# Optimization experiments

Hardware: AMD Instinct MI355X
Metric: run time of the kernel (lower is better)

The kernel has to match this reference:

```python
import jax, jax.numpy as jnp
import numpy as np

B, S, D = 2, 1024, 1024
L, E, F = 2, 8, 2048


def setup_inputs() -> dict:
    key = jax.random.key(0)
    kx, kp, k1, k2 = jax.random.split(key, 4)
    x = jax.random.normal(kx, (B, S, D), dtype=jnp.float32)
    # prototypes scaled so dot products are O(1), keeping softmax well-behaved
    protos = jax.random.normal(kp, (L, E, D), dtype=jnp.float32) / np.sqrt(D)
    W1 = jax.random.normal(k1, (L, E, D, F), dtype=jnp.float32) * 0.02
    W2 = jax.random.normal(k2, (L, E, F, D), dtype=jnp.float32) * 0.02
    return {"x": x, "protos": protos, "W1": W1, "W2": W2, "k": 2}


def _route(x, protos_l, k):
    # expert_mapping: abs(dot(prototype, input)) per expert, keep top-k, rest -> -inf, softmax
    scores = jnp.abs(jnp.einsum("bsd,ed->bse", x, protos_l))  # [B,S,E]
    topv, _ = jax.lax.top_k(scores, k)
    thresh = topv[..., -1:]  # k-th largest per token
    masked = jnp.where(scores >= thresh, scores, -jnp.inf)
    return jax.nn.softmax(masked, axis=-1)  # [B,S,E]


def reference(x, protos, W1, W2, k):
    n_layers = protos.shape[0]
    for l in range(n_layers):  # fixed small layer loop
        w = _route(x, protos[l], k)  # [B,S,E]
        h = jax.nn.relu(jnp.einsum("bsd,edf->bsef", x, W1[l]))  # [B,S,E,F]
        y = jnp.einsum("bsef,efd,bse->bsd", h, W2[l], w)  # weighted expert mix
        x = x + y
    return x
```

## Files before the change

kernel.cpp:

```cpp
#include <hip/hip_runtime.h>
#include <hip/hip_bf16.h>
#include <cstdint>

#define T_TOKENS 2048
#define DDIM 1024
#define FDIM 2048
#define NEXP 8
#define BMPAD 64
#define RMAX 4608
#define RALLOC 4736

#define ATILE_EL 2048
#define BTILE_EL 4096
#define WLDP 132

typedef unsigned short u16;
typedef short bf16x8 __attribute__((ext_vector_type(8)));
typedef u16 u16x8 __attribute__((ext_vector_type(8)));
typedef u16 u16x4v __attribute__((ext_vector_type(4)));
typedef float f32x4 __attribute__((ext_vector_type(4)));

#define VMCNT(n) asm volatile("s_waitcnt vmcnt(" #n ")" ::: "memory")
#define SB() __builtin_amdgcn_sched_barrier(0)
#define BAR() __builtin_amdgcn_s_barrier()

__device__ __forceinline__ u16 bf16_rn(float f) {
  unsigned u = __builtin_bit_cast(unsigned, f);
  u += 0x7fffu + ((u >> 16) & 1u);
  return (u16)(u >> 16);
}
__device__ __forceinline__ float bf16_f(u16 h) {
  unsigned u = ((unsigned)h) << 16;
  return __builtin_bit_cast(float, u);
}
__device__ __forceinline__ void gl16(const void* g, void* l) {
  __builtin_amdgcn_global_load_lds((const __attribute__((address_space(1))) void*)g,
                                   (__attribute__((address_space(3))) void*)l, 16, 0, 0);
}

template <int GX, int GY, int GZ>
__device__ __forceinline__ void swz3(unsigned lin, int& bx, int& by, int& bz) {
  constexpr unsigned nwg = (unsigned)GX * GY * GZ;
  const unsigned nl = (lin & 7u) * (nwg >> 3) + (lin >> 3);
  bx = nl % GX;
  const unsigned t = nl / GX;
  by = t % GY;
  bz = t / GY;
}


__device__ __forceinline__ void route_dev(
    int t, const float* __restrict__ x, const float* __restrict__ protos,
    int* __restrict__ eid, float* __restrict__ wgt, float* red) {
  const int tid = threadIdx.x;
  const float4 xv = ((const float4*)(x + (size_t)t * DDIM))[tid];
  float acc[NEXP];
#pragma unroll
  for (int e = 0; e < NEXP; ++e) {
    const float4 p = ((const float4*)protos)[e * 256 + tid];
    acc[e] = xv.x * p.x + xv.y * p.y + xv.z * p.z + xv.w * p.w;
  }
#pragma unroll
  for (int e = 0; e < NEXP; ++e) red[e * 256 + tid] = acc[e];
  __syncthreads();
  for (int s = 128; s > 0; s >>= 1) {
    if (tid < s) {
#pragma unroll
      for (int e = 0; e < NEXP; ++e) red[e * 256 + tid] += red[e * 256 + tid + s];
    }
    __syncthreads();
  }
  if (tid == 0) {
    float m1 = -1.f, m2 = -1.f;
    int i1 = 0, i2 = 0;
#pragma unroll
    for (int e = 0; e < NEXP; ++e) {
      float s = fabsf(red[e * 256]);
      if (s > m1) { m2 = m1; i2 = i1; m1 = s; i1 = e; }
      else if (s > m2) { m2 = s; i2 = e; }
    }
    float e2 = __expf(m2 - m1);
    float z = 1.f + e2;
    eid[t * 2] = i1;
    eid[t * 2 + 1] = i2;
    wgt[t * 2] = 1.f / z;
    wgt[t * 2 + 1] = e2 / z;
  }
}

template <bool LO>
__device__ __forceinline__ void wconv_dev(
    int nb, int kb, int e, const float* __restrict__ W, u16* __restrict__ Hi,
    u16* __restrict__ Lo, int K, int N, float* tile) {
  const float* Wp = W + ((size_t)e * K + (size_t)kb * 32) * N + nb * 128;
  const int t = threadIdx.x;
#pragma unroll
  for (int i = 0; i < 4; ++i) {
    const int f4 = i * 256 + t;
    const int kr = f4 >> 5;
    const int c4 = (f4 & 31) * 4;
    float4 v = *(const float4*)(Wp + (size_t)kr * N + c4);
    *(float4*)&tile[kr * WLDP + c4] = v;
  }
  __syncthreads();
  const size_t tb = (((size_t)e * (N >> 7) + nb) * (K >> 5) + kb) * BTILE_EL;
#pragma unroll
  for (int j = 0; j < 2; ++j) {
    const int cid = j * 256 + t;
    const int n = cid & 127, ksel = cid >> 7;
    u16x8 hv, lv;
#pragma unroll
    for (int i = 0; i < 8; ++i) {
      float f = tile[(ksel * 8 + i) * WLDP + n];
      u16 h = bf16_rn(f);
      hv[i] = h;
      if (LO) lv[i] = bf16_rn(f - bf16_f(h));
    }
    *(u16x8*)(Hi + tb + (size_t)cid * 8) = hv;
    if (LO) *(u16x8*)(Lo + tb + (size_t)cid * 8) = lv;
  }
}

__device__ __forceinline__ void wconv_p_dev(
    int nb, int kb, int e, const float* __restrict__ W, u16* __restrict__ Hi,
    const float* __restrict__ proto2, float* __restrict__ Ppart, int K, int N,
    float* smem) {
  float* tile = smem;
  float* pr = smem + 32 * WLDP;
  const float* Wp = W + ((size_t)e * K + (size_t)kb * 32) * N + nb * 128;
  const int t = threadIdx.x;
#pragma unroll
  for (int i = 0; i < 4; ++i) {
    const int f4 = i * 256 + t;
    const int kr = f4 >> 5;
    const int c4 = (f4 & 31) * 4;
    float4 v = *(const float4*)(Wp + (size_t)kr * N + c4);
    *(float4*)&tile[kr * WLDP + c4] = v;
  }
  {
    const int idx = t * 4;
    const int e2 = idx >> 7, n = idx & 127;
    *(float4*)&pr[e2 * 128 + n] =
        *(const float4*)(proto2 + (size_t)e2 * DDIM + nb * 128 + n);
  }
  __syncthreads();
  const size_t tb = (((size_t)e * (N >> 7) + nb) * (K >> 5) + kb) * BTILE_EL;
#pragma unroll
  for (int j = 0; j < 2; ++j) {
    const int cid = j * 256 + t;
    const int n = cid & 127, ksel = cid >> 7;
    u16x8 hv;
#pragma unroll
    for (int i = 0; i < 8; ++i) hv[i] = bf16_rn(tile[(ksel * 8 + i) * WLDP + n]);
    *(u16x8*)(Hi + tb + (size_t)cid * 8) = hv;
  }
  const int e2 = t >> 5, f = t & 31;
  float s = 0.f;
#pragma unroll
  for (int ii = 0; ii < 32; ++ii) {
    const int n4 = ((ii + f) & 31) * 4;
    const float4 tv = *(const float4*)&tile[f * WLDP + n4];
    const float4 pv = *(const float4*)&pr[e2 * 128 + n4];
    s += tv.x * pv.x + tv.y * pv.y + tv.z * pv.z + tv.w * pv.w;
  }
  Ppart[(((size_t)nb * NEXP + e) * NEXP + e2) * FDIM + kb * 32 + f] = s;
}

template <bool LO>
__device__ __forceinline__ void gather_dev(
    int r, const float* __restrict__ x, const int* __restrict__ row2token,
    u16* __restrict__ Ahi, u16* __restrict__ Alo) {
  const int t = row2token[r];
  const int c = threadIdx.x * 4;
  float4 v = make_float4(0.f, 0.f, 0.f, 0.f);
  if (t >= 0) v = *(const float4*)(x + (size_t)t * DDIM + c);
  float vv[4] = {v.x, v.y, v.z, v.w};
  u16x4v hi, lo;
#pragma unroll
  for (int i = 0; i < 4; ++i) {
    u16 h = bf16_rn(vv[i]);
    hi[i] = h;
    if (LO) lo[i] = bf16_rn(vv[i] - bf16_f(h));
  }
  const size_t el = ((size_t)(r >> 6) * (DDIM >> 5) + (c >> 5)) * ATILE_EL +
                    (size_t)(((c >> 3) & 3) * 64 + (r & 63)) * 8 + (c & 7);
  *(u16x4v*)(Ahi + el) = hi;
  if (LO) *(u16x4v*)(Alo + el) = lo;
}

__device__ __forceinline__ void route2_dev(
    int t, const float* __restrict__ x, const float* __restrict__ protos2,
    const u16* __restrict__ h_hi, const u16* __restrict__ h_lo,
    const float* __restrict__ P, const int* __restrict__ eidA,
    const int* __restrict__ pos, const float* __restrict__ wgtA,
    int* __restrict__ eidB, float* __restrict__ wgtB, float* red) {
  const int tid = threadIdx.x;
  const float4 xv = ((const float4*)(x + (size_t)t * DDIM))[tid];
  float acc[NEXP];
#pragma unroll
  for (int e = 0; e < NEXP; ++e) {
    const float4 p = ((const float4*)protos2)[e * 256 + tid];
    acc[e] = xv.x * p.x + xv.y * p.y + xv.z * p.z + xv.w * p.w;
  }
  const int p0 = pos[t * 2], p1 = pos[t * 2 + 1];
  const int e0 = eidA[t * 2], e1 = eidA[t * 2 + 1];
  const float w0 = wgtA[t * 2], w1 = wgtA[t * 2 + 1];
  const int f0 = tid * 8;
  const int nkbF = FDIM >> 5;
  float h0[8], h1[8];
  {
    const size_t el0 = ((size_t)(p0 >> 6) * nkbF + (f0 >> 5)) * ATILE_EL +
                       (size_t)((((f0 >> 3) & 3) * 64 + (p0 & 63)) * 8);
    const size_t el1 = ((size_t)(p1 >> 6) * nkbF + (f0 >> 5)) * ATILE_EL +
                       (size_t)((((f0 >> 3) & 3) * 64 + (p1 & 63)) * 8);
    u16x8 a = *(const u16x8*)&h_hi[el0], b = *(const u16x8*)&h_lo[el0];
    u16x8 c = *(const u16x8*)&h_hi[el1], d = *(const u16x8*)&h_lo[el1];
#pragma unroll
    for (int j = 0; j < 8; ++j) {
      h0[j] = bf16_f(a[j]) + bf16_f(b[j]);
      h1[j] = bf16_f(c[j]) + bf16_f(d[j]);
    }
  }
#pragma unroll
  for (int e2 = 0; e2 < NEXP; ++e2) {
    const float* P0 = P + ((size_t)(e0 * NEXP + e2)) * FDIM + f0;
    const float* P1 = P + ((size_t)(e1 * NEXP + e2)) * FDIM + f0;
    float c = 0.f;
#pragma unroll
    for (int j = 0; j < 8; ++j) c += w0 * h0[j] * P0[j] + w1 * h1[j] * P1[j];
    acc[e2] += c;
  }
#pragma unroll
  for (int e = 0; e < NEXP; ++e) red[e * 256 + tid] = acc[e];
  __syncthreads();
  for (int s = 128; s > 0; s >>= 1) {
    if (tid < s) {
#pragma unroll
      for (int e = 0; e < NEXP; ++e) red[e * 256 + tid] += red[e * 256 + tid + s];
    }
    __syncthreads();
  }
  if (tid == 0) {
    float m1 = -1.f, m2 = -1.f;
    int i1 = 0, i2 = 0;
#pragma unroll
    for (int e = 0; e < NEXP; ++e) {
      float s = fabsf(red[e * 256]);
      if (s > m1) { m2 = m1; i2 = i1; m1 = s; i1 = e; }
      else if (s > m2) { m2 = s; i2 = e; }
    }
    float e2 = __expf(m2 - m1);
    float z = 1.f + e2;
    eidB[t * 2] = i1;
    eidB[t * 2 + 1] = i2;
    wgtB[t * 2] = 1.f / z;
    wgtB[t * 2 + 1] = e2 / z;
  }
}

__device__ __forceinline__ void gemm_split_dev(
    unsigned lin, u16* lds, const u16* __restrict__ Ahi, const u16* __restrict__ Alo,
    const u16* __restrict__ Bhi, const u16* __restrict__ Blo,
    u16* __restrict__ OutHi, u16* __restrict__ OutLo,
    const int* __restrict__ cnt, const int* __restrict__ offp, int K, int N) {
  int bx, by, bz;
  swz3<FDIM / 128, RMAX / 64, NEXP>(lin, bx, by, bz);
  const int e = bz;
  const int cp = (cnt[e] + 63) & ~63;
  if (by * 64 >= cp) return;
  const int row0 = offp[e] + by * 64;
  const int n0 = bx * 128;
  const int nkb = K >> 5;
  constexpr int BUF_EL = 12288;

  const int tid = threadIdx.x;
  const int lane = tid & 63;
  const int wid = tid >> 6;
  const int wr = wid >> 1, wc = wid & 1;
  const int lr = lane & 15, kg = lane >> 4;
  const int lo16 = lane << 4;

  f32x4 acc[2][4];
#pragma unroll
  for (int i = 0; i < 2; ++i)
#pragma unroll
    for (int j = 0; j < 4; ++j)
#pragma unroll
      for (int r = 0; r < 4; ++r) acc[i][j][r] = 0.f;

  const size_t abase = (size_t)(row0 >> 6) * nkb;
  const size_t bbase = ((size_t)e * (N >> 7) + (n0 >> 7)) * nkb;

  auto STAGE = [&](int kb, int b) {
    char* d = (char*)(lds + b * BUF_EL);
    const char* gah = (const char*)(Ahi + (abase + kb) * ATILE_EL);
    const char* gal = (const char*)(Alo + (abase + kb) * ATILE_EL);
    const char* gbh = (const char*)(Bhi + (bbase + kb) * BTILE_EL);
    const char* gbl = (const char*)(Blo + (bbase + kb) * BTILE_EL);
    if (wid == 0) {
      gl16(gah + 0 * 1024 + lo16, d + 0 * 1024);
      gl16(gah + 1 * 1024 + lo16, d + 1 * 1024);
      gl16(gah + 2 * 1024 + lo16, d + 2 * 1024);
      gl16(gah + 3 * 1024 + lo16, d + 3 * 1024);
      gl16(gal + 0 * 1024 + lo16, d + 4096 + 0 * 1024);
      gl16(gal + 1 * 1024 + lo16, d + 4096 + 1 * 1024);
    } else if (wid == 1) {
      gl16(gal + 2 * 1024 + lo16, d + 4096 + 2 * 1024);
      gl16(gal + 3 * 1024 + lo16, d + 4096 + 3 * 1024);
      gl16(gbh + 0 * 1024 + lo16, d + 8192 + 0 * 1024);
      gl16(gbh + 1 * 1024 + lo16, d + 8192 + 1 * 1024);
      gl16(gbh + 2 * 1024 + lo16, d + 8192 + 2 * 1024);
      gl16(gbh + 3 * 1024 + lo16, d + 8192 + 3 * 1024);
    } else if (wid == 2) {
      gl16(gbh + 4 * 1024 + lo16, d + 8192 + 4 * 1024);
      gl16(gbh + 5 * 1024 + lo16, d + 8192 + 5 * 1024);
      gl16(gbh + 6 * 1024 + lo16, d + 8192 + 6 * 1024);
      gl16(gbh + 7 * 1024 + lo16, d + 8192 + 7 * 1024);
      gl16(gbl + 0 * 1024 + lo16, d + 16384 + 0 * 1024);
      gl16(gbl + 1 * 1024 + lo16, d + 16384 + 1 * 1024);
    } else {
      gl16(gbl + 2 * 1024 + lo16, d + 16384 + 2 * 1024);
      gl16(gbl + 3 * 1024 + lo16, d + 16384 + 3 * 1024);
      gl16(gbl + 4 * 1024 + lo16, d + 16384 + 4 * 1024);
      gl16(gbl + 5 * 1024 + lo16, d + 16384 + 5 * 1024);
      gl16(gbl + 6 * 1024 + lo16, d + 16384 + 6 * 1024);
      gl16(gbl + 7 * 1024 + lo16, d + 16384 + 7 * 1024);
    }
  };

  STAGE(0, 0);
  int cur = 0;
  for (int kb = 0; kb < nkb; ++kb) {
    const bool pf = (kb + 1 < nkb);
    if (pf) STAGE(kb + 1, cur ^ 1);
    if (pf) { VMCNT(6); } else { VMCNT(0); }
    SB(); BAR(); SB();

    const u16* buf = lds + cur * BUF_EL;
    const u16* AsH = buf;
    const u16* AsL = buf + 2048;
    const u16* BsH = buf + 4096;
    const u16* BsL = buf + 8192;
    const int arow = (kg * 64 + wr * 32 + lr) * 8;
    const int bcol = (kg * 128 + wc * 64 + lr) * 8;

    bf16x8 ah0 = *(const bf16x8*)&AsH[arow];
    bf16x8 ah1 = *(const bf16x8*)&AsH[arow + 128];
    bf16x8 bh[4];
#pragma unroll
    for (int j = 0; j < 4; ++j) bh[j] = *(const bf16x8*)&BsH[bcol + j * 128];
#pragma unroll
    for (int j = 0; j < 4; ++j) {
      acc[0][j] = __builtin_amdgcn_mfma_f32_16x16x32_bf16(ah0, bh[j], acc[0][j], 0, 0, 0);
      acc[1][j] = __builtin_amdgcn_mfma_f32_16x16x32_bf16(ah1, bh[j], acc[1][j], 0, 0, 0);
    }
    bf16x8 al0 = *(const bf16x8*)&AsL[arow];
    bf16x8 al1 = *(const bf16x8*)&AsL[arow + 128];
#pragma unroll
    for (int j = 0; j < 4; ++j) {
      bf16x8 bl = *(const bf16x8*)&BsL[bcol + j * 128];
      acc[0][j] = __builtin_amdgcn_mfma_f32_16x16x32_bf16(ah0, bl, acc[0][j], 0, 0, 0);
      acc[1][j] = __builtin_amdgcn_mfma_f32_16x16x32_bf16(ah1, bl, acc[1][j], 0, 0, 0);
      acc[0][j] = __builtin_amdgcn_mfma_f32_16x16x32_bf16(al0, bh[j], acc[0][j], 0, 0, 0);
      acc[1][j] = __builtin_amdgcn_mfma_f32_16x16x32_bf16(al1, bh[j], acc[1][j], 0, 0, 0);
    }
    SB(); BAR(); SB();
    cur ^= 1;
  }

  const int nkbO = N >> 5;
#pragma unroll
  for (int i = 0; i < 2; ++i) {
#pragma unroll
    for (int j = 0; j < 4; ++j) {
      const int Cj = n0 + wc * 64 + j * 16 + lr;
      f32x4 v = acc[i][j];
#pragma unroll
      for (int r = 0; r < 4; ++r) {
        const int R = row0 + wr * 32 + i * 16 + kg * 4 + r;
        float f = fmaxf(v[r], 0.f);
        const size_t el = ((size_t)(R >> 6) * nkbO + (Cj >> 5)) * ATILE_EL +
                          (size_t)(((Cj >> 3) & 3) * 64 + (R & 63)) * 8 + (Cj & 7);
        u16 h = bf16_rn(f);
        OutHi[el] = h;
        OutLo[el] = bf16_rn(f - bf16_f(h));
      }
    }
  }
}

template <int GX, int GY, bool RELU, int OUTMODE>
__device__ __forceinline__ void gemm_plain_dev(
    unsigned lin, u16* lds, const u16* __restrict__ Ahi, const u16* __restrict__ Bhi,
    u16* __restrict__ OutHi, float* __restrict__ OutF,
    const int* __restrict__ cnt, const int* __restrict__ offp, int K, int N) {
  int bx, by, bz;
  swz3<GX, GY, NEXP>(lin, bx, by, bz);
  const int e = bz;
  const int cp = (cnt[e] + 63) & ~63;
  if (by * 128 >= cp) return;
  const int row0 = offp[e] + by * 128;
  const int rend = offp[e] + cp;
  const int n0 = bx * 128;
  const int nkb = K >> 5;
  constexpr int BUF_EL = 8192;

  const int tid = threadIdx.x;
  const int lane = tid & 63;
  const int wid = tid >> 6;
  const int wr = wid >> 1, wc = wid & 1;
  const int lr = lane & 15, kg = lane >> 4;
  const int lo16 = lane << 4;

  f32x4 acc[4][4];
#pragma unroll
  for (int i = 0; i < 4; ++i)
#pragma unroll
    for (int j = 0; j < 4; ++j)
#pragma unroll
      for (int r = 0; r < 4; ++r) acc[i][j][r] = 0.f;

  const int at0 = row0 >> 6;
  const size_t bbase = ((size_t)e * (N >> 7) + (n0 >> 7)) * nkb;

  auto STAGE = [&](int kb, int b) {
    char* d = (char*)(lds + b * BUF_EL);
    if (wid < 2) {
      const char* g = (const char*)(Ahi + ((size_t)(at0 + wid) * nkb + kb) * ATILE_EL);
      gl16(g + 0 * 1024 + lo16, d + wid * 4096 + 0 * 1024);
      gl16(g + 1 * 1024 + lo16, d + wid * 4096 + 1 * 1024);
      gl16(g + 2 * 1024 + lo16, d + wid * 4096 + 2 * 1024);
      gl16(g + 3 * 1024 + lo16, d + wid * 4096 + 3 * 1024);
    } else {
      const char* g = (const char*)(Bhi + (bbase + kb) * BTILE_EL) + (wid - 2) * 4096;
      gl16(g + 0 * 1024 + lo16, d + 8192 + (wid - 2) * 4096 + 0 * 1024);
      gl16(g + 1 * 1024 + lo16, d + 8192 + (wid - 2) * 4096 + 1 * 1024);
      gl16(g + 2 * 1024 + lo16, d + 8192 + (wid - 2) * 4096 + 2 * 1024);
      gl16(g + 3 * 1024 + lo16, d + 8192 + (wid - 2) * 4096 + 3 * 1024);
    }
  };

  STAGE(0, 0);
  int cur = 0;
  for (int kb = 0; kb < nkb; ++kb) {
    const bool pf = (kb + 1 < nkb);
    if (pf) STAGE(kb + 1, cur ^ 1);
    if (pf) { VMCNT(4); } else { VMCNT(0); }
    SB(); BAR(); SB();

    const u16* buf = lds + cur * BUF_EL;
    const u16* AsH = buf + wr * 2048;
    const u16* BsH = buf + 4096;
    const int arow = (kg * 64 + lr) * 8;
    const int bcol = (kg * 128 + wc * 64 + lr) * 8;

    bf16x8 ah[4], bh[4];
#pragma unroll
    for (int i = 0; i < 4; ++i) ah[i] = *(const bf16x8*)&AsH[arow + i * 128];
#pragma unroll
    for (int j = 0; j < 4; ++j) bh[j] = *(const bf16x8*)&BsH[bcol + j * 128];
#pragma unroll
    for (int i = 0; i < 4; ++i)
#pragma unroll
      for (int j = 0; j < 4; ++j)
        acc[i][j] = __builtin_amdgcn_mfma_f32_16x16x32_bf16(ah[i], bh[j], acc[i][j], 0, 0, 0);
    SB(); BAR(); SB();
    cur ^= 1;
  }

  const int nkbO = N >> 5;
#pragma unroll
  for (int i = 0; i < 4; ++i) {
#pragma unroll
    for (int j = 0; j < 4; ++j) {
      const int Cj = n0 + wc * 64 + j * 16 + lr;
      f32x4 v = acc[i][j];
#pragma unroll
      for (int r = 0; r < 4; ++r) {
        const int R = row0 + wr * 64 + i * 16 + kg * 4 + r;
        if (R >= rend) continue;
        float f = v[r];
        if (RELU) f = fmaxf(f, 0.f);
        if constexpr (OUTMODE == 0) {
          OutF[(size_t)R * N + Cj] = f;
        } else {
          const size_t el = ((size_t)(R >> 6) * nkbO + (Cj >> 5)) * ATILE_EL +
                            (size_t)(((Cj >> 3) & 3) * 64 + (R & 63)) * 8 + (Cj & 7);
          OutHi[el] = bf16_rn(f);
        }
      }
    }
  }
}

__device__ __forceinline__ void compact_dev(
    const int* __restrict__ eid, int* __restrict__ cnt, int* __restrict__ offp,
    int* __restrict__ row2token, int* __restrict__ pos, int* lcnt) {
  int* s_off = lcnt + NEXP * 256;
  int* s_tot = s_off + NEXP;
  const int tid = threadIdx.x;
  const int base = tid * 16;
  int my[16];
#pragma unroll
  for (int i = 0; i < 4; ++i)
    *(int4*)&my[i * 4] = *(const int4*)(eid + base + i * 4);
#pragma unroll
  for (int e = 0; e < NEXP; ++e) {
    int c = 0;
#pragma unroll
    for (int i = 0; i < 16; ++i) c += (my[i] == e) ? 1 : 0;
    lcnt[e * 256 + tid] = c;
  }
  for (int r = tid; r < RMAX; r += 256) row2token[r] = -1;
  __syncthreads();
  if (tid < NEXP) {
    int run = 0;
    for (int i = 0; i < 256; ++i) {
      int v = lcnt[tid * 256 + i];
      lcnt[tid * 256 + i] = run;
      run += v;
    }
    s_tot[tid] = run;
  }
  __syncthreads();
  if (tid == 0) {
    int o = 0;
    for (int e = 0; e < NEXP; ++e) {
      s_off[e] = o;
      o += (s_tot[e] + BMPAD - 1) & ~(BMPAD - 1);
    }
  }
  __syncthreads();
  int myoff[NEXP];
#pragma unroll
  for (int e = 0; e < NEXP; ++e) myoff[e] = s_off[e] + lcnt[e * 256 + tid];
#pragma unroll
  for (int i = 0; i < 16; ++i) {
    int r = 0;
#pragma unroll
    for (int e = 0; e < NEXP; ++e) r = (my[i] == e) ? myoff[e] : r;
    row2token[r] = (base + i) >> 1;
    pos[base + i] = r;
#pragma unroll
    for (int e = 0; e < NEXP; ++e) myoff[e] += (my[i] == e) ? 1 : 0;
  }
  if (tid < NEXP) {
    cnt[tid] = s_tot[tid];
    offp[tid] = s_off[tid];
  }
}


__global__ __launch_bounds__(256) void fusedK1_kernel(
    const float* __restrict__ xin, const float* __restrict__ protos,
    int* __restrict__ eidA, float* __restrict__ wgtA,
    const float* __restrict__ W2, u16* __restrict__ W2A,
    const float* __restrict__ proto2, float* __restrict__ Ppart,
    const float* __restrict__ W1, u16* __restrict__ W_hi, u16* __restrict__ W_lo) {
  __shared__ float smem[32 * WLDP + 8 * 128];
  const unsigned lin = blockIdx.x;
  if (lin < 2048u) {
    route_dev((int)lin, xin, protos, eidA, wgtA, smem);
  } else if (lin < 6144u) {
    const unsigned l2 = lin - 2048u;
    wconv_p_dev(l2 % 8, (l2 / 8) % 64, l2 / 512, W2, W2A, proto2, Ppart,
                FDIM, DDIM, smem);
  } else {
    const unsigned l3 = lin - 6144u;
    wconv_dev<true>(l3 % 16, (l3 / 16) % 32, l3 / 512, W1, W_hi, W_lo,
                    DDIM, FDIM, smem);
  }
}

__global__ __launch_bounds__(256) void compact_kernel(
    const int* __restrict__ eid, int* __restrict__ cnt, int* __restrict__ offp,
    int* __restrict__ row2token, int* __restrict__ pos) {
  __shared__ int lcnt[NEXP * 256 + 16];
  compact_dev(eid, cnt, offp, row2token, pos, lcnt);
}

__global__ __launch_bounds__(256) void fusedK3_kernel(
    const float* __restrict__ xin, const int* __restrict__ row2token,
    u16* __restrict__ Ag_hi, u16* __restrict__ Ag_lo,
    const float* __restrict__ Ppart, float* __restrict__ P) {
  const unsigned lin = blockIdx.x;
  if (lin < (unsigned)RMAX) {
    gather_dev<true>((int)lin, xin, row2token, Ag_hi, Ag_lo);
  } else {
    const int i = (int)(lin - RMAX) * 256 + threadIdx.x;
    float s = 0.f;
#pragma unroll
    for (int nb = 0; nb < 8; ++nb) s += Ppart[(size_t)nb * (NEXP * NEXP * FDIM) + i];
    P[i] = s;
  }
}

__global__ __launch_bounds__(256, 3) void fusedC2_kernel(
    const u16* __restrict__ Ag_hi, const u16* __restrict__ Ag_lo,
    const u16* __restrict__ W_hi, const u16* __restrict__ W_lo,
    u16* __restrict__ h_hi, u16* __restrict__ h_lo,
    const int* __restrict__ cnt, const int* __restrict__ offp) {
  __shared__ u16 lds[2 * 12288];
  gemm_split_dev(blockIdx.x, lds, Ag_hi, Ag_lo, W_hi, W_lo, h_hi, h_lo, cnt, offp,
                 DDIM, FDIM);
}

__global__ __launch_bounds__(256, 4) void fusedC3_kernel(
    const u16* __restrict__ h_hi, const u16* __restrict__ h_lo,
    const u16* __restrict__ W2A,
    float* __restrict__ part, const int* __restrict__ cnt, const int* __restrict__ offp,
    const float* __restrict__ W1b, u16* __restrict__ W_lo,
    const float* __restrict__ W2b, u16* __restrict__ W_hi,
    const float* __restrict__ xin, const float* __restrict__ protos2,
    const float* __restrict__ P, const int* __restrict__ eidA,
    const int* __restrict__ posA, const float* __restrict__ wgtA,
    int* __restrict__ eidB, float* __restrict__ wgtB) {
  __shared__ u16 lds[2 * 8192];
  const unsigned lin = blockIdx.x;
  if (lin < 2304u) {
    gemm_plain_dev<DDIM / 128, RMAX / 128, false, 0>(
        lin, lds, h_hi, W2A, nullptr, part, cnt, offp, FDIM, DDIM);
  } else if (lin < 6400u) {
    const unsigned l2 = lin - 2304u;
    wconv_dev<false>(l2 % 16, (l2 / 16) % 32, l2 / 512, W1b, W_lo, nullptr,
                     DDIM, FDIM, (float*)lds);
  } else if (lin < 10496u) {
    const unsigned l2 = lin - 6400u;
    wconv_dev<false>(l2 % 8, (l2 / 8) % 64, l2 / 512, W2b, W_hi, nullptr,
                     FDIM, DDIM, (float*)lds);
  } else {
    route2_dev((int)(lin - 10496u), xin, protos2, h_hi, h_lo, P, eidA, posA, wgtA,
               eidB, wgtB, (float*)lds);
  }
}

__global__ __launch_bounds__(256) void fusedD_kernel(
    const float* __restrict__ part, const int* __restrict__ pos,
    const float* __restrict__ wgt, const float* __restrict__ xin,
    float* __restrict__ xcur,
    const int* __restrict__ eidB, int* __restrict__ cnt, int* __restrict__ offp,
    int* __restrict__ row2token, int* __restrict__ posB) {
  __shared__ int lcnt[NEXP * 256 + 16];
  const unsigned lin = blockIdx.x;
  if (lin < 2048u) {
    const int t = lin;
    const int c = threadIdx.x * 4;
    const int p0 = pos[t * 2], p1 = pos[t * 2 + 1];
    const float w0 = wgt[t * 2], w1 = wgt[t * 2 + 1];
    float4 xa = *(const float4*)(xin + (size_t)t * DDIM + c);
    const float4 y0 = *(const float4*)(part + (size_t)p0 * DDIM + c);
    const float4 y1 = *(const float4*)(part + (size_t)p1 * DDIM + c);
    xa.x += w0 * y0.x + w1 * y1.x;
    xa.y += w0 * y0.y + w1 * y1.y;
    xa.z += w0 * y0.z + w1 * y1.z;
    xa.w += w0 * y0.w + w1 * y1.w;
    *(float4*)(xcur + (size_t)t * DDIM + c) = xa;
  } else {
    compact_dev(eidB, cnt, offp, row2token, posB, lcnt);
  }
}

__global__ __launch_bounds__(256) void gather_kernel(
    const float* __restrict__ x, const int* __restrict__ row2token,
    u16* __restrict__ Ahi) {
  gather_dev<false>(blockIdx.x, x, row2token, Ahi, nullptr);
}

template <int GX, bool RELU, int OUTMODE>
__global__ __launch_bounds__(256, 4) void gemm_plain_kernel(
    const u16* __restrict__ Ahi, const u16* __restrict__ Bhi,
    u16* __restrict__ OutHi, float* __restrict__ OutF,
    const int* __restrict__ cnt, const int* __restrict__ offp, int K, int N) {
  __shared__ u16 lds[2 * 8192];
  gemm_plain_dev<GX, RMAX / 128, RELU, OUTMODE>(blockIdx.x, lds, Ahi, Bhi, OutHi,
                                                OutF, cnt, offp, K, N);
}

__global__ __launch_bounds__(256) void apply_kernel(
    const float* __restrict__ part, const int* __restrict__ pos,
    const float* __restrict__ wgt, float* __restrict__ x) {
  const int t = blockIdx.x;
  const int c = threadIdx.x * 4;
  const int p0 = pos[t * 2], p1 = pos[t * 2 + 1];
  const float w0 = wgt[t * 2], w1 = wgt[t * 2 + 1];
  float4 xa = *(float4*)(x + (size_t)t * DDIM + c);
  const float4 y0 = *(const float4*)(part + (size_t)p0 * DDIM + c);
  const float4 y1 = *(const float4*)(part + (size_t)p1 * DDIM + c);
  xa.x += w0 * y0.x + w1 * y1.x;
  xa.y += w0 * y0.y + w1 * y1.y;
  xa.z += w0 * y0.z + w1 * y1.z;
  xa.w += w0 * y0.w + w1 * y1.w;
  *(float4*)(x + (size_t)t * DDIM + c) = xa;
}

extern "C" void kernel_launch(void* const* d_in, const int* in_sizes, int n_in,
                              void* d_out, int out_size, void* d_ws, size_t ws_size,
                              hipStream_t stream) {
  const float* xin = (const float*)d_in[0];
  const float* protos = (const float*)d_in[1];
  const float* W1 = (const float*)d_in[2];
  const float* W2 = (const float*)d_in[3];
  float* xcur = (float*)d_out;

  u16* W_hi = (u16*)d_ws;
  u16* W_lo = W_hi + (size_t)NEXP * DDIM * FDIM;
  u16* W2A = W_lo + (size_t)NEXP * DDIM * FDIM;
  u16* Ag_hi = W2A + (size_t)NEXP * DDIM * FDIM;
  u16* Ag_lo = Ag_hi + (size_t)RALLOC * DDIM;
  u16* h_hi = Ag_lo + (size_t)RALLOC * DDIM;
  u16* h_lo = h_hi + (size_t)RALLOC * FDIM;
  float* part = (float*)(h_lo + (size_t)RALLOC * FDIM);
  float* Ppart = part + (size_t)RALLOC * DDIM;
  float* P = Ppart + (size_t)8 * NEXP * NEXP * FDIM;
  float* wgtA = P + (size_t)NEXP * NEXP * FDIM;
  float* wgtB = wgtA + T_TOKENS * 2;
  int* eidA = (int*)(wgtB + T_TOKENS * 2);
  int* eidB = eidA + T_TOKENS * 2;
  int* posA = eidB + T_TOKENS * 2;
  int* posB = posA + T_TOKENS * 2;
  int* cnt = posB + T_TOKENS * 2;
  int* offp = cnt + NEXP;
  int* row2token = offp + NEXP;

  const float* protos2 = protos + (size_t)NEXP * DDIM;
  const float* W1b = W1 + (size_t)NEXP * DDIM * FDIM;
  const float* W2b = W2 + (size_t)NEXP * FDIM * DDIM;

  fusedK1_kernel<<<2048 + 4096 + 4096, 256, 0, stream>>>(
      xin, protos, eidA, wgtA, W2, W2A, protos2, Ppart, W1, W_hi, W_lo);
  compact_kernel<<<1, 256, 0, stream>>>(eidA, cnt, offp, row2token, posA);
  fusedK3_kernel<<<RMAX + 512, 256, 0, stream>>>(
      xin, row2token, Ag_hi, Ag_lo, Ppart, P);
  fusedC2_kernel<<<(FDIM / 128) * (RMAX / 64) * NEXP, 256, 0, stream>>>(
      Ag_hi, Ag_lo, W_hi, W_lo, h_hi, h_lo, cnt, offp);
  fusedC3_kernel<<<2304 + 4096 + 4096 + 2048, 256, 0, stream>>>(
      h_hi, h_lo, W2A, part, cnt, offp, W1b, W_lo, W2b, W_hi,
      xin, protos2, P, eidA, posA, wgtA, eidB, wgtB);
  fusedD_kernel<<<2048 + 1, 256, 0, stream>>>(
      part, posA, wgtA, xin, xcur, eidB, cnt, offp, row2token, posB);

  gather_kernel<<<RMAX, 256, 0, stream>>>(xcur, row2token, Ag_hi);
  gemm_plain_kernel<FDIM / 128, true, 2>
      <<<(FDIM / 128) * (RMAX / 128) * NEXP, 256, 0, stream>>>(
          Ag_hi, W_lo, h_hi, nullptr, cnt, offp, DDIM, FDIM);
  gemm_plain_kernel<DDIM / 128, false, 0>
      <<<(DDIM / 128) * (RMAX / 128) * NEXP, 256, 0, stream>>>(
          h_hi, W_hi, nullptr, part, cnt, offp, FDIM, DDIM);
  apply_kernel<<<T_TOKENS, 256, 0, stream>>>(part, posB, wgtB, xcur);
}
```

Before: 315.3 us.

## Enlarge split-bf16 first-layer GEMM tile to 128 rows and reorder MFMAs

The split hi/lo bf16 GEMM for the first layer now computes a 128x128 output tile instead of 64x128. Each wave handles 64 rows with a 4x4 accumulator array, and the grid is halved. This reuses the B tiles across twice as many rows, which cuts global and LDS traffic per FLOP. The cost is more LDS and registers and lower occupancy (launch bounds drop to 2), a row guard on the output for experts whose count is padded only to 64, and possible reads of stale A rows past the padded end. A small LDS bank-rotation tweak in the prototype dot-product loop is also included.

```diff
diff --git a/kernel.cpp b/kernel.cpp
--- a/kernel.cpp
+++ b/kernel.cpp
@@ -158,7 +158,7 @@
   float s = 0.f;
 #pragma unroll
   for (int ii = 0; ii < 32; ++ii) {
-    const int n4 = ((ii + f) & 31) * 4;
+    const int n4 = ((ii + 2 * f) & 31) * 4;
     const float4 tv = *(const float4*)&tile[f * WLDP + n4];
     const float4 pv = *(const float4*)&pr[e2 * 128 + n4];
     s += tv.x * pv.x + tv.y * pv.y + tv.z * pv.z + tv.w * pv.w;
@@ -264,14 +264,15 @@
     u16* __restrict__ OutHi, u16* __restrict__ OutLo,
     const int* __restrict__ cnt, const int* __restrict__ offp, int K, int N) {
   int bx, by, bz;
-  swz3<FDIM / 128, RMAX / 64, NEXP>(lin, bx, by, bz);
+  swz3<FDIM / 128, RMAX / 128, NEXP>(lin, bx, by, bz);
   const int e = bz;
   const int cp = (cnt[e] + 63) & ~63;
-  if (by * 64 >= cp) return;
-  const int row0 = offp[e] + by * 64;
+  if (by * 128 >= cp) return;
+  const int row0 = offp[e] + by * 128;
+  const int rend = offp[e] + cp;
   const int n0 = bx * 128;
   const int nkb = K >> 5;
-  constexpr int BUF_EL = 12288;
+  constexpr int BUF_EL = 16384;
 
   const int tid = threadIdx.x;
   const int lane = tid & 63;
@@ -280,51 +281,61 @@
   const int lr = lane & 15, kg = lane >> 4;
   const int lo16 = lane << 4;
 
-  f32x4 acc[2][4];
-#pragma unroll
-  for (int i = 0; i < 2; ++i)
+  f32x4 acc[4][4];
+#pragma unroll
+  for (int i = 0; i < 4; ++i)
 #pragma unroll
     for (int j = 0; j < 4; ++j)
 #pragma unroll
       for (int r = 0; r < 4; ++r) acc[i][j][r] = 0.f;
 
-  const size_t abase = (size_t)(row0 >> 6) * nkb;
+  const int at0 = row0 >> 6;
   const size_t bbase = ((size_t)e * (N >> 7) + (n0 >> 7)) * nkb;
 
   auto STAGE = [&](int kb, int b) {
     char* d = (char*)(lds + b * BUF_EL);
-    const char* gah = (const char*)(Ahi + (abase + kb) * ATILE_EL);
-    const char* gal = (const char*)(Alo + (abase + kb) * ATILE_EL);
-    const char* gbh = (const char*)(Bhi + (bbase + kb) * BTILE_EL);
-    const char* gbl = (const char*)(Blo + (bbase + kb) * BTILE_EL);
     if (wid == 0) {
-      gl16(gah + 0 * 1024 + lo16, d + 0 * 1024);
-      gl16(gah + 1 * 1024 + lo16, d + 1 * 1024);
-      gl16(gah + 2 * 1024 + lo16, d + 2 * 1024);
-      gl16(gah + 3 * 1024 + lo16, d + 3 * 1024);
-      gl16(gal + 0 * 1024 + lo16, d + 4096 + 0 * 1024);
-      gl16(gal + 1 * 1024 + lo16, d + 4096 + 1 * 1024);
+      const char* g0 = (const char*)(Ahi + ((size_t)at0 * nkb + kb) * ATILE_EL);
+      const char* g1 = (const char*)(Ahi + ((size_t)(at0 + 1) * nkb + kb) * ATILE_EL);
+      gl16(g0 + 0 * 1024 + lo16, d + 0 * 1024);
+      gl16(g0 + 1 * 1024 + lo16, d + 1 * 1024);
+      gl16(g0 + 2 * 1024 + lo16, d + 2 * 1024);
+      gl16(g0 + 3 * 1024 + lo16, d + 3 * 1024);
+      gl16(g1 + 0 * 1024 + lo16, d + 4096 + 0 * 1024);
+      gl16(g1 + 1 * 1024 + lo16, d + 4096 + 1 * 1024);
+      gl16(g1 + 2 * 1024 + lo16, d + 4096 + 2 * 1024);
+      gl16(g1 + 3 * 1024 + lo16, d + 4096 + 3 * 1024);
     } else if (wid == 1) {
-      gl16(gal + 2 * 1024 + lo16, d + 4096 + 2 * 1024);
-      gl16(gal + 3 * 1024 + lo16, d + 4096 + 3 * 1024);
-      gl16(gbh + 0 * 1024 + lo16, d + 8192 + 0 * 1024);
-      gl16(gbh + 1 * 1024 + lo16, d + 8192 + 1 * 1024);
-      gl16(gbh + 2 * 1024 + lo16, d + 8192 + 2 * 1024);
-      gl16(gbh + 3 * 1024 + lo16, d + 8192 + 3 * 1024);
+      const char* g0 = (const char*)(Alo + ((size_t)at0 * nkb + kb) * ATILE_EL);
+      const char* g1 = (const char*)(Alo + ((size_t)(at0 + 1) * nkb + kb) * ATILE_EL);
+      gl16(g0 + 0 * 1024 + lo16, d + 8192 + 0 * 1024);
+      gl16(g0 + 1 * 1024 + lo16, d + 8192 + 1 * 1024);
+      gl16(g0 + 2 * 1024 + lo16, d + 8192 + 2 * 1024);
+      gl16(g0 + 3 * 1024 + lo16, d + 8192 + 3 * 1024);
+      gl16(g1 + 0 * 1024 + lo16, d + 12288 + 0 * 1024);
+      gl16(g1 + 1 * 1024 + lo16, d + 12288 + 1 * 1024);
+      gl16(g1 + 2 * 1024 + lo16, d + 12288 + 2 * 1024);
+      gl16(g1 + 3 * 1024 + lo16, d + 12288 + 3 * 1024);
     } else if (wid == 2) {
-      gl16(gbh + 4 * 1024 + lo16, d + 8192 + 4 * 1024);
-      gl16(gbh + 5 * 1024 + lo16, d + 8192 + 5 * 1024);
-      gl16(gbh + 6 * 1024 + lo16, d + 8192 + 6 * 1024);
-      gl16(gbh + 7 * 1024 + lo16, d + 8192 + 7 * 1024);
-      gl16(gbl + 0 * 1024 + lo16, d + 16384 + 0 * 1024);
-      gl16(gbl + 1 * 1024 + lo16, d + 16384 + 1 * 1024);
+      const char* g = (const char*)(Bhi + (bbase + kb) * BTILE_EL);
+      gl16(g + 0 * 1024 + lo16, d + 16384 + 0 * 1024);
+      gl16(g + 1 * 1024 + lo16, d + 16384 + 1 * 1024);
+      gl16(g + 2 * 1024 + lo16, d + 16384 + 2 * 1024);
+      gl16(g + 3 * 1024 + lo16, d + 16384 + 3 * 1024);
+      gl16(g + 4 * 1024 + lo16, d + 16384 + 4 * 1024);
+      gl16(g + 5 * 1024 + lo16, d + 16384 + 5 * 1024);
+      gl16(g + 6 * 1024 + lo16, d + 16384 + 6 * 1024);
+      gl16(g + 7 * 1024 + lo16, d + 16384 + 7 * 1024);
     } else {
-      gl16(gbl + 2 * 1024 + lo16, d + 16384 + 2 * 1024);
-      gl16(gbl + 3 * 1024 + lo16, d + 16384 + 3 * 1024);
-      gl16(gbl + 4 * 1024 + lo16, d + 16384 + 4 * 1024);
-      gl16(gbl + 5 * 1024 + lo16, d + 16384 + 5 * 1024);
-      gl16(gbl + 6 * 1024 + lo16, d + 16384 + 6 * 1024);
-      gl16(gbl + 7 * 1024 + lo16, d + 16384 + 7 * 1024);
+      const char* g = (const char*)(Blo + (bbase + kb) * BTILE_EL);
+      gl16(g + 0 * 1024 + lo16, d + 24576 + 0 * 1024);
+      gl16(g + 1 * 1024 + lo16, d + 24576 + 1 * 1024);
+      gl16(g + 2 * 1024 + lo16, d + 24576 + 2 * 1024);
+      gl16(g + 3 * 1024 + lo16, d + 24576 + 3 * 1024);
+      gl16(g + 4 * 1024 + lo16, d + 24576 + 4 * 1024);
+      gl16(g + 5 * 1024 + lo16, d + 24576 + 5 * 1024);
+      gl16(g + 6 * 1024 + lo16, d + 24576 + 6 * 1024);
+      gl16(g + 7 * 1024 + lo16, d + 24576 + 7 * 1024);
     }
   };
 
@@ -333,51 +344,58 @@
   for (int kb = 0; kb < nkb; ++kb) {
     const bool pf = (kb + 1 < nkb);
     if (pf) STAGE(kb + 1, cur ^ 1);
-    if (pf) { VMCNT(6); } else { VMCNT(0); }
+    if (pf) { VMCNT(8); } else { VMCNT(0); }
     SB(); BAR(); SB();
 
     const u16* buf = lds + cur * BUF_EL;
-    const u16* AsH = buf;
-    const u16* AsL = buf + 2048;
-    const u16* BsH = buf + 4096;
-    const u16* BsL = buf + 8192;
-    const int arow = (kg * 64 + wr * 32 + lr) * 8;
+    const u16* AsH = buf + wr * 2048;
+    const u16* AsL = buf + 4096 + wr * 2048;
+    const u16* BsH = buf + 8192;
+    const u16* BsL = buf + 12288;
+    const int arow = (kg * 64 + lr) * 8;
     const int bcol = (kg * 128 + wc * 64 + lr) * 8;
 
-    bf16x8 ah0 = *(const bf16x8*)&AsH[arow];
-    bf16x8 ah1 = *(const bf16x8*)&AsH[arow + 128];
-    bf16x8 bh[4];
+    bf16x8 ah[4], bh[4];
+#pragma unroll
+    for (int i = 0; i < 4; ++i) ah[i] = *(const bf16x8*)&AsH[arow + i * 128];
 #pragma unroll
     for (int j = 0; j < 4; ++j) bh[j] = *(const bf16x8*)&BsH[bcol + j * 128];
 #pragma unroll
-    for (int j = 0; j < 4; ++j) {
-      acc[0][j] = __builtin_amdgcn_mfma_f32_16x16x32_bf16(ah0, bh[j], acc[0][j], 0, 0, 0);
-      acc[1][j] = __builtin_amdgcn_mfma_f32_16x16x32_bf16(ah1, bh[j], acc[1][j], 0, 0, 0);
-    }
-    bf16x8 al0 = *(const bf16x8*)&AsL[arow];
-    bf16x8 al1 = *(const bf16x8*)&AsL[arow + 128];
-#pragma unroll
-    for (int j = 0; j < 4; ++j) {
-      bf16x8 bl = *(const bf16x8*)&BsL[bcol + j * 128];
-      acc[0][j] = __builtin_amdgcn_mfma_f32_16x16x32_bf16(ah0, bl, acc[0][j], 0, 0, 0);
-      acc[1][j] = __builtin_amdgcn_mfma_f32_16x16x32_bf16(ah1, bl, acc[1][j], 0, 0, 0);
-      acc[0][j] = __builtin_amdgcn_mfma_f32_16x16x32_bf16(al0, bh[j], acc[0][j], 0, 0, 0);
-      acc[1][j] = __builtin_amdgcn_mfma_f32_16x16x32_bf16(al1, bh[j], acc[1][j], 0, 0, 0);
-    }
+    for (int i = 0; i < 4; ++i)
+#pragma unroll
+      for (int j = 0; j < 4; ++j)
+        acc[i][j] = __builtin_amdgcn_mfma_f32_16x16x32_bf16(ah[i], bh[j], acc[i][j], 0, 0, 0);
+    bf16x8 bl[4];
+#pragma unroll
+    for (int j = 0; j < 4; ++j) bl[j] = *(const bf16x8*)&BsL[bcol + j * 128];
+#pragma unroll
+    for (int i = 0; i < 4; ++i)
+#pragma unroll
+      for (int j = 0; j < 4; ++j)
+        acc[i][j] = __builtin_amdgcn_mfma_f32_16x16x32_bf16(ah[i], bl[j], acc[i][j], 0, 0, 0);
+    bf16x8 al[4];
+#pragma unroll
+    for (int i = 0; i < 4; ++i) al[i] = *(const bf16x8*)&AsL[arow + i * 128];
+#pragma unroll
+    for (int i = 0; i < 4; ++i)
+#pragma unroll
+      for (int j = 0; j < 4; ++j)
+        acc[i][j] = __builtin_amdgcn_mfma_f32_16x16x32_bf16(al[i], bh[j], acc[i][j], 0, 0, 0);
     SB(); BAR(); SB();
     cur ^= 1;
   }
 
   const int nkbO = N >> 5;
 #pragma unroll
-  for (int i = 0; i < 2; ++i) {
+  for (int i = 0; i < 4; ++i) {
 #pragma unroll
     for (int j = 0; j < 4; ++j) {
       const int Cj = n0 + wc * 64 + j * 16 + lr;
       f32x4 v = acc[i][j];
 #pragma unroll
       for (int r = 0; r < 4; ++r) {
-        const int R = row0 + wr * 32 + i * 16 + kg * 4 + r;
+        const int R = row0 + wr * 64 + i * 16 + kg * 4 + r;
+        if (R >= rend) continue;
         float f = fmaxf(v[r], 0.f);
         const size_t el = ((size_t)(R >> 6) * nkbO + (Cj >> 5)) * ATILE_EL +
                           (size_t)(((Cj >> 3) & 3) * 64 + (R & 63)) * 8 + (Cj & 7);
@@ -595,12 +613,12 @@
   }
 }
 
-__global__ __launch_bounds__(256, 3) void fusedC2_kernel(
+__global__ __launch_bounds__(256, 2) void fusedC2_kernel(
     const u16* __restrict__ Ag_hi, const u16* __restrict__ Ag_lo,
     const u16* __restrict__ W_hi, const u16* __restrict__ W_lo,
     u16* __restrict__ h_hi, u16* __restrict__ h_lo,
     const int* __restrict__ cnt, const int* __restrict__ offp) {
-  __shared__ u16 lds[2 * 12288];
+  __shared__ u16 lds[2 * 16384];
   gemm_split_dev(blockIdx.x, lds, Ag_hi, Ag_lo, W_hi, W_lo, h_hi, h_lo, cnt, offp,
                  DDIM, FDIM);
 }
@@ -731,7 +749,7 @@
   compact_kernel<<<1, 256, 0, stream>>>(eidA, cnt, offp, row2token, posA);
   fusedK3_kernel<<<RMAX + 512, 256, 0, stream>>>(
       xin, row2token, Ag_hi, Ag_lo, Ppart, P);
-  fusedC2_kernel<<<(FDIM / 128) * (RMAX / 64) * NEXP, 256, 0, stream>>>(
+  fusedC2_kernel<<<(FDIM / 128) * (RMAX / 128) * NEXP, 256, 0, stream>>>(
       Ag_hi, Ag_lo, W_hi, W_lo, h_hi, h_lo, cnt, offp);
   fusedC3_kernel<<<2304 + 4096 + 4096 + 2048, 256, 0, stream>>>(
       h_hi, h_lo, W2A, part, cnt, offp, W1b, W_lo, W2b, W_hi,
```

Measured after the change: 334.6 us. 1.06x slower.
